# Kernel tuning notes

Hardware: AMD Instinct MI355X
Metric: run time of the kernel (lower is better)

The kernel has to match this reference:

```python
import jax, jax.numpy as jnp
import numpy as np

C_M, C_Z, C_H = 256, 128, 32
EPS = 1e-3      # outer-product-mean normalization eps
LN_EPS = 1e-5   # LayerNorm eps (torch default)


def setup_inputs() -> dict:
    key = jax.random.key(0)
    ks = jax.random.split(key, 8)
    B, S, R = 1, 128, 256
    m = jax.random.normal(ks[0], (B, S, R, C_M), dtype=jnp.float32)
    mask = jnp.ones((B, S, R), dtype=jnp.float32)
    ln_g = jnp.ones((C_M,), dtype=jnp.float32)
    ln_b = jnp.zeros((C_M,), dtype=jnp.float32)
    w1 = jax.random.normal(ks[1], (C_M, C_H), dtype=jnp.float32) * (1.0 / np.sqrt(C_M))
    b1 = jnp.zeros((C_H,), dtype=jnp.float32)
    w2 = jax.random.normal(ks[2], (C_M, C_H), dtype=jnp.float32) * (1.0 / np.sqrt(C_M))
    b2 = jnp.zeros((C_H,), dtype=jnp.float32)
    # linear_out uses init='final' (zeros) in training; use small random for a nontrivial baseline
    w_out = jax.random.normal(ks[3], (C_H * C_H, C_Z), dtype=jnp.float32) * 0.02
    b_out = jnp.zeros((C_Z,), dtype=jnp.float32)
    return {"m": m, "mask": mask, "ln_g": ln_g, "ln_b": ln_b,
            "w1": w1, "b1": b1, "w2": w2, "b2": b2,
            "w_out": w_out, "b_out": b_out}


def reference(m, mask, ln_g, ln_b, w1, b1, w2, b2, w_out, b_out):
    # LayerNorm over c_m
    mu = jnp.mean(m, axis=-1, keepdims=True)
    var = jnp.mean(jnp.square(m - mu), axis=-1, keepdims=True)
    mn = (m - mu) * jax.lax.rsqrt(var + LN_EPS) * ln_g + ln_b

    msk = mask[..., None]                       # [B,S,R,1]
    a = (mn @ w1 + b1) * msk                    # [B,S,R,h]
    b = (mn @ w2 + b2) * msk                    # [B,S,R,h]
    a = jnp.swapaxes(a, -2, -3)                 # [B,R,S,h]
    b = jnp.swapaxes(b, -2, -3)                 # [B,R,S,h]

    # outer product mean over the MSA (seq) dim: [B,R,R,h,h]
    outer = jnp.einsum('...isc,...jse->...ijce', a, b)
    outer = outer.reshape(*outer.shape[:-2], C_H * C_H)  # [B,R,R,h*h]
    outer = outer @ w_out + b_out               # [B,R,R,c_z]

    # normalization: pairwise count of valid MSA rows
    norm = jnp.einsum('...sia,...sja->...ija', msk, msk)  # [B,R,R,1]
    return outer / (EPS + norm)
```

## Files before the change

kernel.cpp:

```cpp
#include <hip/hip_runtime.h>

#define R   256
#define S   128
#define CM  256
#define CH  32
#define CZ  128

typedef __attribute__((ext_vector_type(8))) short short8;
typedef __attribute__((ext_vector_type(4))) float f32x4;
typedef unsigned short ushort_t;

__device__ inline ushort_t f2bf(float f) {
    union { float f; unsigned u; } v; v.f = f;
    unsigned u = v.u;
    unsigned r = u + 0x7FFF + ((u >> 16) & 1);
    return (ushort_t)(r >> 16);
}

__global__ __launch_bounds__(256) void k_prep(
    const float* __restrict__ mask, const float* __restrict__ w_out,
    const float* __restrict__ w1, const float* __restrict__ w2,
    float* __restrict__ scale, ushort_t* __restrict__ WTp,
    ushort_t* __restrict__ WcatT) {
    __shared__ float red[4][64];
    int b = blockIdx.x, t = threadIdx.x;
    if (b < 1024) {
        int i = b >> 2, jq = b & 3;
        int jl = t & 63, wv = t >> 6;
        int j = jq * 64 + jl;
        const float* mi = mask + (size_t)(wv * 32) * R + i;
        const float* mj = mask + (size_t)(wv * 32) * R + j;
        float acc = 0.f;
        #pragma unroll
        for (int s = 0; s < 32; ++s) acc += mi[s * R] * mj[s * R];
        red[wv][jl] = acc;
        __syncthreads();
        if (t < 64) {
            float v = red[0][t] + red[1][t] + red[2][t] + red[3][t];
            scale[(size_t)i * R + jq * 64 + t] = 1.0f / (1e-3f + v);
        }
    } else if (b < 1152) {
        int z = b - 1024;
        #pragma unroll
        for (int q = 0; q < 4; ++q) {
            int k2 = q * 256 + t;
            int e = k2 >> 5, c = k2 & 31;
            WTp[(size_t)z * 1024 + k2] = f2bf(w_out[(size_t)(c * 32 + e) * CZ + z]);
        }
    } else {
        int ch = b - 1152, k = t;
        const float* w = (ch < CH) ? w1 : w2;
        WcatT[(size_t)ch * CM + k] = f2bf(w[(size_t)k * CH + (ch & 31)]);
    }
}

__global__ __launch_bounds__(256) void k_lnproj(
    const float* __restrict__ m, const float* __restrict__ mask,
    const float* __restrict__ g, const float* __restrict__ beta,
    const float* __restrict__ b1, const float* __restrict__ b2,
    const ushort_t* __restrict__ WcatT,
    ushort_t* __restrict__ Abig, ushort_t* __restrict__ BbigT) {
    __shared__ ushort_t mnL[64 * CM];
    int t = threadIdx.x;
    int sg = blockIdx.x & 7, rg = blockIdx.x >> 3;
    int s0 = sg * 16, r0 = rg * 4;

    int ml = t >> 2, part = t & 3;
    int r_l = ml >> 4, s_l = ml & 15;
    size_t p = (size_t)(s0 + s_l) * R + (r0 + r_l);
    const float4* row = (const float4*)(m + p * CM + part * 64);
    float4 x[16];
    float sum = 0.f, sq = 0.f;
    #pragma unroll
    for (int i = 0; i < 16; ++i) {
        x[i] = row[i];
        sum += x[i].x + x[i].y + x[i].z + x[i].w;
        sq  += x[i].x * x[i].x + x[i].y * x[i].y
             + x[i].z * x[i].z + x[i].w * x[i].w;
    }
    sum += __shfl_xor(sum, 1); sum += __shfl_xor(sum, 2);
    sq  += __shfl_xor(sq, 1);  sq  += __shfl_xor(sq, 2);
    float mean = sum * (1.0f / CM);
    float var  = sq * (1.0f / CM) - mean * mean;
    float inv  = rsqrtf(var + 1e-5f);
    const float4* g4 = (const float4*)(g + part * 64);
    const float4* be4 = (const float4*)(beta + part * 64);
    #pragma unroll
    for (int c8 = 0; c8 < 8; ++c8) {
        float4 a = x[2 * c8], b = x[2 * c8 + 1];
        float4 ga = g4[2 * c8], gb = g4[2 * c8 + 1];
        float4 ba = be4[2 * c8], bb = be4[2 * c8 + 1];
        union { ushort_t u[8]; uint4 v; } pk;
        pk.u[0] = f2bf((a.x - mean) * inv * ga.x + ba.x);
        pk.u[1] = f2bf((a.y - mean) * inv * ga.y + ba.y);
        pk.u[2] = f2bf((a.z - mean) * inv * ga.z + ba.z);
        pk.u[3] = f2bf((a.w - mean) * inv * ga.w + ba.w);
        pk.u[4] = f2bf((b.x - mean) * inv * gb.x + bb.x);
        pk.u[5] = f2bf((b.y - mean) * inv * gb.y + bb.y);
        pk.u[6] = f2bf((b.z - mean) * inv * gb.z + bb.z);
        pk.u[7] = f2bf((b.w - mean) * inv * gb.w + bb.w);
        int ck = part * 8 + c8;
        int phys = ck ^ (ml & 15);
        *(uint4*)&mnL[ml * CM + phys * 8] = pk.v;
    }

    int w = t >> 6, lane = t & 63, quad = lane >> 4, l15 = lane & 15;
    int ch = w * 16 + l15;
    short8 bfrs[8];
    #pragma unroll
    for (int ks = 0; ks < 8; ++ks)
        bfrs[ks] = *(const short8*)&WcatT[(size_t)ch * CM + (ks * 4 + quad) * 8];
    __syncthreads();

    f32x4 acc[4];
    #pragma unroll
    for (int a = 0; a < 4; a++) acc[a] = (f32x4)(0.f);
    #pragma unroll
    for (int ks = 0; ks < 8; ++ks) {
        int cb = ks * 4 + quad;
        #pragma unroll
        for (int mt = 0; mt < 4; ++mt) {
            int mm = mt * 16 + l15;
            short8 afr = *(const short8*)&mnL[mm * CM + ((cb ^ l15) << 3)];
            acc[mt] = __builtin_amdgcn_mfma_f32_16x16x32_bf16(afr, bfrs[ks], acc[mt], 0, 0, 0);
        }
    }

    int c = ch & 31;
    float bias = (ch < CH) ? b1[c] : b2[c];
    ushort_t* dst = (ch < CH) ? Abig : BbigT;
    #pragma unroll
    for (int mt = 0; mt < 4; ++mt) {
        int r = r0 + mt;
        union { ushort_t u[4]; uint2 v; } pk;
        #pragma unroll
        for (int reg = 0; reg < 4; ++reg) {
            int s = s0 + quad * 4 + reg;
            float mv = mask[(size_t)s * R + r];
            pk.u[reg] = f2bf((acc[mt][reg] + bias) * mv);
        }
        *(uint2*)&dst[((size_t)r * CH + c) * S + s0 + quad * 4] = pk.v;
    }
}

__global__ __launch_bounds__(512, 4) void k_fuse(
    const ushort_t* __restrict__ Abig, const ushort_t* __restrict__ BbigT,
    const ushort_t* __restrict__ WTp, const float* __restrict__ b_out,
    const float* __restrict__ scale, float* __restrict__ out) {
    __shared__ ushort_t oc[64 * 128];
    __shared__ ushort_t shB[2][32 * 128];
    int t = threadIdx.x;
    int w = t >> 6, lane = t & 63, quad = lane >> 4, l15 = lane & 15;
    int ib = blockIdx.x >> 5, jb = blockIdx.x & 31;
    int i_g = ib * 8 + w;
    int jj = l15 & 7, elb = l15 >> 3;

    short8 af[2][4];
    #pragma unroll
    for (int mt = 0; mt < 2; ++mt)
        #pragma unroll
        for (int ks = 0; ks < 4; ++ks)
            af[mt][ks] = *(const short8*)
                &Abig[((size_t)i_g * 32 + mt * 16 + l15) * S + ks * 32 + quad * 8];

    int r2 = t >> 4, ck = t & 15;
    const ushort_t* gB = BbigT
        + ((size_t)jb * 256 + (r2 & 7) * 32 + (r2 >> 3)) * S + ck * 8;
    ushort_t* bdst[2];
    bdst[0] = &shB[0][r2 * 128 + ((ck ^ (r2 & 15)) << 3)];
    bdst[1] = &shB[1][r2 * 128 + ((ck ^ (r2 & 15)) << 3)];
    uint4 breg = *(const uint4*)&gB[0];

    const ushort_t* Wp = WTp + (size_t)(w * 16 + l15) * 1024 + quad * 8;
    short8 wcur[4], wnxt[4];
    #pragma unroll
    for (int k = 0; k < 4; ++k) wcur[k] = *(const short8*)&Wp[k * 32];

    int pwr = w * 8 + jj;

    f32x4 acc2[4];
    #pragma unroll
    for (int pt = 0; pt < 4; ++pt) acc2[pt] = (f32x4)(0.f);

    for (int ec = 0; ec < 8; ++ec) {
        int buf = ec & 1;
        *(uint4*)bdst[buf] = breg;
        __syncthreads();

        if (ec < 7) {
            breg = *(const uint4*)&gB[(ec + 1) * 512];
            #pragma unroll
            for (int k = 0; k < 4; ++k)
                wnxt[k] = *(const short8*)&Wp[(ec + 1) * 128 + k * 32];
        }

        f32x4 acc1[2][2];
        #pragma unroll
        for (int a = 0; a < 2; a++)
            #pragma unroll
            for (int b = 0; b < 2; b++) acc1[a][b] = (f32x4)(0.f);
        #pragma unroll
        for (int ks = 0; ks < 4; ++ks) {
            int chq = ks * 4 + quad;
            int r20 = elb * 8 + jj;
            int r21 = r20 + 16;
            short8 bf0 = *(const short8*)
                &shB[buf][r20 * 128 + ((chq ^ (r20 & 15)) << 3)];
            short8 bf1 = *(const short8*)
                &shB[buf][r21 * 128 + ((chq ^ (r21 & 15)) << 3)];
            #pragma unroll
            for (int mt = 0; mt < 2; ++mt) {
                acc1[mt][0] = __builtin_amdgcn_mfma_f32_16x16x32_bf16(
                    af[mt][ks], bf0, acc1[mt][0], 0, 0, 0);
                acc1[mt][1] = __builtin_amdgcn_mfma_f32_16x16x32_bf16(
                    af[mt][ks], bf1, acc1[mt][1], 0, 0, 0);
            }
        }
        #pragma unroll
        for (int mt = 0; mt < 2; ++mt) {
            int c00 = mt * 16 + quad * 4;
            #pragma unroll
            for (int nt = 0; nt < 2; ++nt) {
                int el = nt * 2 + elb;
                int k2l = el * 32 + c00;
                int cc = k2l >> 3;
                union { ushort_t u[4]; uint2 v; } pk;
                #pragma unroll
                for (int reg = 0; reg < 4; ++reg)
                    pk.u[reg] = f2bf(acc1[mt][nt][reg]);
                *(uint2*)((char*)oc + pwr * 256 + ((cc ^ (pwr & 7)) << 4)
                          + ((k2l & 7) << 1)) = pk.v;
            }
        }
        __syncthreads();
        #pragma unroll
        for (int ksl = 0; ksl < 4; ++ksl) {
            short8 wf = wcur[ksl];
            #pragma unroll
            for (int pt = 0; pt < 4; ++pt) {
                int pp = pt * 16 + l15;
                int cc = ksl * 4 + quad;
                short8 of = *(const short8*)
                    ((const char*)oc + pp * 256 + ((cc ^ (pp & 7)) << 4));
                acc2[pt] = __builtin_amdgcn_mfma_f32_16x16x32_bf16(
                    of, wf, acc2[pt], 0, 0, 0);
            }
        }
        #pragma unroll
        for (int k = 0; k < 4; ++k) wcur[k] = wnxt[k];
    }

    float bz = b_out[w * 16 + l15];
    #pragma unroll
    for (int pt = 0; pt < 4; ++pt) {
        #pragma unroll
        for (int reg = 0; reg < 4; ++reg) {
            int pp = pt * 16 + quad * 4 + reg;
            int pg = (ib * 8 + (pp >> 3)) * R + jb * 8 + (pp & 7);
            out[(size_t)pg * CZ + w * 16 + l15] = (acc2[pt][reg] + bz) * scale[pg];
        }
    }
}

extern "C" void kernel_launch(void* const* d_in, const int* in_sizes, int n_in,
                              void* d_out, int out_size, void* d_ws, size_t ws_size,
                              hipStream_t stream) {
    const float* m    = (const float*)d_in[0];
    const float* mask = (const float*)d_in[1];
    const float* g    = (const float*)d_in[2];
    const float* be   = (const float*)d_in[3];
    const float* w1   = (const float*)d_in[4];
    const float* b1   = (const float*)d_in[5];
    const float* w2   = (const float*)d_in[6];
    const float* b2   = (const float*)d_in[7];
    const float* wo   = (const float*)d_in[8];
    const float* bo   = (const float*)d_in[9];
    float* out = (float*)d_out;

    char* ws = (char*)d_ws;
    ushort_t* Abig  = (ushort_t*)ws;
    ushort_t* BbigT = Abig + (size_t)R * CH * S;
    ushort_t* WTp   = BbigT + (size_t)R * CH * S;
    ushort_t* WcatT = WTp + (size_t)CZ * CH * CH;
    float*    scale = (float*)(WcatT + (size_t)64 * CM);

    k_prep<<<1216, 256, 0, stream>>>(mask, wo, w1, w2, scale, WTp, WcatT);
    k_lnproj<<<512, 256, 0, stream>>>(m, mask, g, be, b1, b2, WcatT, Abig, BbigT);
    k_fuse<<<1024, 512, 0, stream>>>(Abig, BbigT, WTp, bo, scale, out);
}
```

Measured before the change: 158.3 us.

## Restructure fused outer-product GEMM tiling and fold mask-norm/W_out prep into lnproj

The mask-count normalization and w_out transpose work moves out of the prep kernel into extra blocks of the LN/projection kernel, so the first launch shrinks to a tiny w1/w2 conversion. In the fused kernel, B fragments are now loaded directly from global memory into registers instead of being staged through shared memory. The outer-product staging buffer is double-buffered, and the second GEMM is retiled so each wave computes 32 rows by 32 output channels with W fragments streamed from global memory. The 4-blocks-per-SM occupancy hint is dropped. The aim is fewer barriers and less LDS traffic, at the cost of more global loads and higher register pressure.

```diff
diff --git a/kernel.cpp b/kernel.cpp
--- a/kernel.cpp
+++ b/kernel.cpp
@@ -17,15 +17,39 @@
     return (ushort_t)(r >> 16);
 }
 
-__global__ __launch_bounds__(256) void k_prep(
-    const float* __restrict__ mask, const float* __restrict__ w_out,
+__global__ __launch_bounds__(256) void k_prepW(
     const float* __restrict__ w1, const float* __restrict__ w2,
-    float* __restrict__ scale, ushort_t* __restrict__ WTp,
     ushort_t* __restrict__ WcatT) {
-    __shared__ float red[4][64];
-    int b = blockIdx.x, t = threadIdx.x;
-    if (b < 1024) {
-        int i = b >> 2, jq = b & 3;
+    int ch = blockIdx.x, k = threadIdx.x;
+    const float* w = (ch < CH) ? w1 : w2;
+    WcatT[(size_t)ch * CM + k] = f2bf(w[(size_t)k * CH + (ch & 31)]);
+}
+
+__global__ __launch_bounds__(256) void k_lnproj(
+    const float* __restrict__ m, const float* __restrict__ mask,
+    const float* __restrict__ g, const float* __restrict__ beta,
+    const float* __restrict__ b1, const float* __restrict__ b2,
+    const ushort_t* __restrict__ WcatT, const float* __restrict__ w_out,
+    ushort_t* __restrict__ Abig, ushort_t* __restrict__ BbigT,
+    float* __restrict__ scale, ushort_t* __restrict__ WTp) {
+    __shared__ ushort_t mnL[64 * CM];
+    int t = threadIdx.x;
+    int b = blockIdx.x;
+
+    if (b >= 1536) {
+        int z = b - 1536;
+        #pragma unroll
+        for (int q = 0; q < 4; ++q) {
+            int k2 = q * 256 + t;
+            int e = k2 >> 5, c = k2 & 31;
+            WTp[(size_t)z * 1024 + k2] = f2bf(w_out[(size_t)(c * 32 + e) * CZ + z]);
+        }
+        return;
+    }
+    if (b >= 512) {
+        float* red = (float*)mnL;
+        int bb = b - 512;
+        int i = bb >> 2, jq = bb & 3;
         int jl = t & 63, wv = t >> 6;
         int j = jq * 64 + jl;
         const float* mi = mask + (size_t)(wv * 32) * R + i;
@@ -33,36 +57,16 @@
         float acc = 0.f;
         #pragma unroll
         for (int s = 0; s < 32; ++s) acc += mi[s * R] * mj[s * R];
-        red[wv][jl] = acc;
+        red[wv * 64 + jl] = acc;
         __syncthreads();
         if (t < 64) {
-            float v = red[0][t] + red[1][t] + red[2][t] + red[3][t];
+            float v = red[t] + red[64 + t] + red[128 + t] + red[192 + t];
             scale[(size_t)i * R + jq * 64 + t] = 1.0f / (1e-3f + v);
         }
-    } else if (b < 1152) {
-        int z = b - 1024;
-        #pragma unroll
-        for (int q = 0; q < 4; ++q) {
-            int k2 = q * 256 + t;
-            int e = k2 >> 5, c = k2 & 31;
-            WTp[(size_t)z * 1024 + k2] = f2bf(w_out[(size_t)(c * 32 + e) * CZ + z]);
-        }
-    } else {
-        int ch = b - 1152, k = t;
-        const float* w = (ch < CH) ? w1 : w2;
-        WcatT[(size_t)ch * CM + k] = f2bf(w[(size_t)k * CH + (ch & 31)]);
-    }
-}
-
-__global__ __launch_bounds__(256) void k_lnproj(
-    const float* __restrict__ m, const float* __restrict__ mask,
-    const float* __restrict__ g, const float* __restrict__ beta,
-    const float* __restrict__ b1, const float* __restrict__ b2,
-    const ushort_t* __restrict__ WcatT,
-    ushort_t* __restrict__ Abig, ushort_t* __restrict__ BbigT) {
-    __shared__ ushort_t mnL[64 * CM];
-    int t = threadIdx.x;
-    int sg = blockIdx.x & 7, rg = blockIdx.x >> 3;
+        return;
+    }
+
+    int sg = b & 7, rg = b >> 3;
     int s0 = sg * 16, r0 = rg * 4;
 
     int ml = t >> 2, part = t & 3;
@@ -87,7 +91,7 @@
     const float4* be4 = (const float4*)(beta + part * 64);
     #pragma unroll
     for (int c8 = 0; c8 < 8; ++c8) {
-        float4 a = x[2 * c8], b = x[2 * c8 + 1];
+        float4 a = x[2 * c8], bq = x[2 * c8 + 1];
         float4 ga = g4[2 * c8], gb = g4[2 * c8 + 1];
         float4 ba = be4[2 * c8], bb = be4[2 * c8 + 1];
         union { ushort_t u[8]; uint4 v; } pk;
@@ -95,10 +99,10 @@
         pk.u[1] = f2bf((a.y - mean) * inv * ga.y + ba.y);
         pk.u[2] = f2bf((a.z - mean) * inv * ga.z + ba.z);
         pk.u[3] = f2bf((a.w - mean) * inv * ga.w + ba.w);
-        pk.u[4] = f2bf((b.x - mean) * inv * gb.x + bb.x);
-        pk.u[5] = f2bf((b.y - mean) * inv * gb.y + bb.y);
-        pk.u[6] = f2bf((b.z - mean) * inv * gb.z + bb.z);
-        pk.u[7] = f2bf((b.w - mean) * inv * gb.w + bb.w);
+        pk.u[4] = f2bf((bq.x - mean) * inv * gb.x + bb.x);
+        pk.u[5] = f2bf((bq.y - mean) * inv * gb.y + bb.y);
+        pk.u[6] = f2bf((bq.z - mean) * inv * gb.z + bb.z);
+        pk.u[7] = f2bf((bq.w - mean) * inv * gb.w + bb.w);
         int ck = part * 8 + c8;
         int phys = ck ^ (ml & 15);
         *(uint4*)&mnL[ml * CM + phys * 8] = pk.v;
@@ -143,12 +147,11 @@
     }
 }
 
-__global__ __launch_bounds__(512, 4) void k_fuse(
+__global__ __launch_bounds__(512) void k_fuse(
     const ushort_t* __restrict__ Abig, const ushort_t* __restrict__ BbigT,
     const ushort_t* __restrict__ WTp, const float* __restrict__ b_out,
     const float* __restrict__ scale, float* __restrict__ out) {
-    __shared__ ushort_t oc[64 * 128];
-    __shared__ ushort_t shB[2][32 * 128];
+    __shared__ ushort_t oc[2][64 * 128];
     int t = threadIdx.x;
     int w = t >> 6, lane = t & 63, quad = lane >> 4, l15 = lane & 15;
     int ib = blockIdx.x >> 5, jb = blockIdx.x & 31;
@@ -163,57 +166,41 @@
             af[mt][ks] = *(const short8*)
                 &Abig[((size_t)i_g * 32 + mt * 16 + l15) * S + ks * 32 + quad * 8];
 
-    int r2 = t >> 4, ck = t & 15;
-    const ushort_t* gB = BbigT
-        + ((size_t)jb * 256 + (r2 & 7) * 32 + (r2 >> 3)) * S + ck * 8;
-    ushort_t* bdst[2];
-    bdst[0] = &shB[0][r2 * 128 + ((ck ^ (r2 & 15)) << 3)];
-    bdst[1] = &shB[1][r2 * 128 + ((ck ^ (r2 & 15)) << 3)];
-    uint4 breg = *(const uint4*)&gB[0];
-
-    const ushort_t* Wp = WTp + (size_t)(w * 16 + l15) * 1024 + quad * 8;
-    short8 wcur[4], wnxt[4];
-    #pragma unroll
-    for (int k = 0; k < 4; ++k) wcur[k] = *(const short8*)&Wp[k * 32];
-
+    const ushort_t* gB = BbigT + ((size_t)jb * 256 + jj * 32 + elb) * S + quad * 8;
+
+    const ushort_t* Wp = WTp + ((size_t)((w & 3) * 32) + l15) * 1024 + quad * 8;
+
+    int ph = w >> 2;
     int pwr = w * 8 + jj;
 
-    f32x4 acc2[4];
-    #pragma unroll
-    for (int pt = 0; pt < 4; ++pt) acc2[pt] = (f32x4)(0.f);
-
+    f32x4 acc2[2][2];
+    #pragma unroll
+    for (int a = 0; a < 2; ++a)
+        #pragma unroll
+        for (int zt = 0; zt < 2; ++zt) acc2[a][zt] = (f32x4)(0.f);
+
+    short8 bcur[2][4];
+    #pragma unroll
+    for (int nt = 0; nt < 2; ++nt)
+        #pragma unroll
+        for (int ks = 0; ks < 4; ++ks)
+            bcur[nt][ks] = *(const short8*)&gB[(size_t)(nt * 2) * S + ks * 32];
+
+    #pragma unroll
     for (int ec = 0; ec < 8; ++ec) {
-        int buf = ec & 1;
-        *(uint4*)bdst[buf] = breg;
-        __syncthreads();
-
-        if (ec < 7) {
-            breg = *(const uint4*)&gB[(ec + 1) * 512];
-            #pragma unroll
-            for (int k = 0; k < 4; ++k)
-                wnxt[k] = *(const short8*)&Wp[(ec + 1) * 128 + k * 32];
-        }
-
         f32x4 acc1[2][2];
         #pragma unroll
         for (int a = 0; a < 2; a++)
             #pragma unroll
-            for (int b = 0; b < 2; b++) acc1[a][b] = (f32x4)(0.f);
+            for (int bq = 0; bq < 2; bq++) acc1[a][bq] = (f32x4)(0.f);
         #pragma unroll
         for (int ks = 0; ks < 4; ++ks) {
-            int chq = ks * 4 + quad;
-            int r20 = elb * 8 + jj;
-            int r21 = r20 + 16;
-            short8 bf0 = *(const short8*)
-                &shB[buf][r20 * 128 + ((chq ^ (r20 & 15)) << 3)];
-            short8 bf1 = *(const short8*)
-                &shB[buf][r21 * 128 + ((chq ^ (r21 & 15)) << 3)];
             #pragma unroll
             for (int mt = 0; mt < 2; ++mt) {
                 acc1[mt][0] = __builtin_amdgcn_mfma_f32_16x16x32_bf16(
-                    af[mt][ks], bf0, acc1[mt][0], 0, 0, 0);
+                    af[mt][ks], bcur[0][ks], acc1[mt][0], 0, 0, 0);
                 acc1[mt][1] = __builtin_amdgcn_mfma_f32_16x16x32_bf16(
-                    af[mt][ks], bf1, acc1[mt][1], 0, 0, 0);
+                    af[mt][ks], bcur[1][ks], acc1[mt][1], 0, 0, 0);
             }
         }
         #pragma unroll
@@ -228,36 +215,52 @@
                 #pragma unroll
                 for (int reg = 0; reg < 4; ++reg)
                     pk.u[reg] = f2bf(acc1[mt][nt][reg]);
-                *(uint2*)((char*)oc + pwr * 256 + ((cc ^ (pwr & 7)) << 4)
-                          + ((k2l & 7) << 1)) = pk.v;
+                *(uint2*)((char*)oc[ec & 1] + pwr * 256
+                          + ((cc ^ (pwr & 15)) << 4) + ((k2l & 7) << 1)) = pk.v;
             }
         }
         __syncthreads();
+
+        if (ec < 7) {
+            #pragma unroll
+            for (int nt = 0; nt < 2; ++nt)
+                #pragma unroll
+                for (int ks = 0; ks < 4; ++ks)
+                    bcur[nt][ks] = *(const short8*)
+                        &gB[(size_t)((ec + 1) * 4 + nt * 2) * S + ks * 32];
+        }
+
         #pragma unroll
         for (int ksl = 0; ksl < 4; ++ksl) {
-            short8 wf = wcur[ksl];
-            #pragma unroll
-            for (int pt = 0; pt < 4; ++pt) {
-                int pp = pt * 16 + l15;
-                int cc = ksl * 4 + quad;
+            short8 wf0 = *(const short8*)&Wp[ec * 128 + ksl * 32];
+            short8 wf1 = *(const short8*)&Wp[16 * 1024 + ec * 128 + ksl * 32];
+            #pragma unroll
+            for (int mtile = 0; mtile < 2; ++mtile) {
+                int pp = ph * 32 + mtile * 16 + l15;
+                int cc2 = ksl * 4 + quad;
                 short8 of = *(const short8*)
-                    ((const char*)oc + pp * 256 + ((cc ^ (pp & 7)) << 4));
-                acc2[pt] = __builtin_amdgcn_mfma_f32_16x16x32_bf16(
-                    of, wf, acc2[pt], 0, 0, 0);
+                    ((const char*)oc[ec & 1] + pp * 256 + ((cc2 ^ (pp & 15)) << 4));
+                acc2[mtile][0] = __builtin_amdgcn_mfma_f32_16x16x32_bf16(
+                    of, wf0, acc2[mtile][0], 0, 0, 0);
+                acc2[mtile][1] = __builtin_amdgcn_mfma_f32_16x16x32_bf16(
+                    of, wf1, acc2[mtile][1], 0, 0, 0);
             }
         }
-        #pragma unroll
-        for (int k = 0; k < 4; ++k) wcur[k] = wnxt[k];
-    }
-
-    float bz = b_out[w * 16 + l15];
-    #pragma unroll
-    for (int pt = 0; pt < 4; ++pt) {
+    }
+
+    float bz0 = b_out[(w & 3) * 32 + l15];
+    float bz1 = b_out[(w & 3) * 32 + 16 + l15];
+    #pragma unroll
+    for (int mtile = 0; mtile < 2; ++mtile) {
         #pragma unroll
         for (int reg = 0; reg < 4; ++reg) {
-            int pp = pt * 16 + quad * 4 + reg;
-            int pg = (ib * 8 + (pp >> 3)) * R + jb * 8 + (pp & 7);
-            out[(size_t)pg * CZ + w * 16 + l15] = (acc2[pt][reg] + bz) * scale[pg];
+            int pq = ph * 32 + mtile * 16 + quad * 4 + reg;
+            int pg = (ib * 8 + (pq >> 3)) * R + jb * 8 + (pq & 7);
+            float sc = scale[pg];
+            out[(size_t)pg * CZ + (w & 3) * 32 + l15]
+                = (acc2[mtile][0][reg] + bz0) * sc;
+            out[(size_t)pg * CZ + (w & 3) * 32 + 16 + l15]
+                = (acc2[mtile][1][reg] + bz1) * sc;
         }
     }
 }
@@ -284,7 +287,8 @@
     ushort_t* WcatT = WTp + (size_t)CZ * CH * CH;
     float*    scale = (float*)(WcatT + (size_t)64 * CM);
 
-    k_prep<<<1216, 256, 0, stream>>>(mask, wo, w1, w2, scale, WTp, WcatT);
-    k_lnproj<<<512, 256, 0, stream>>>(m, mask, g, be, b1, b2, WcatT, Abig, BbigT);
+    k_prepW<<<64, 256, 0, stream>>>(w1, w2, WcatT);
+    k_lnproj<<<1664, 256, 0, stream>>>(m, mask, g, be, b1, b2, WcatT, wo,
+                                       Abig, BbigT, scale, WTp);
     k_fuse<<<1024, 512, 0, stream>>>(Abig, BbigT, WTp, bo, scale, out);
 }
```

After: 238.6 us. 50.7% more time.

## Fold prep kernel into LN-projection launch and load fused weights directly

Applied to the files above, without the earlier changes.

Merges the mask-count, w_out transpose and LN+projection work into one launch by dispatching on block index, which removes one kernel launch and its dependency gap. The separate w1/w2 transposed bf16 copy is dropped; each LN block now converts the projection weights from fp32 with strided global reads. In the fused kernel the register double-buffer for w_out fragments is removed in favour of direct loads inside the loop. This saves registers but may expose load latency, and the strided per-block weight conversion adds redundant global traffic.

```diff
diff --git a/kernel.cpp b/kernel.cpp
--- a/kernel.cpp
+++ b/kernel.cpp
@@ -17,15 +17,32 @@
     return (ushort_t)(r >> 16);
 }
 
-__global__ __launch_bounds__(256) void k_prep(
-    const float* __restrict__ mask, const float* __restrict__ w_out,
+__global__ __launch_bounds__(256) void k_lnproj(
+    const float* __restrict__ m, const float* __restrict__ mask,
+    const float* __restrict__ g, const float* __restrict__ beta,
+    const float* __restrict__ b1, const float* __restrict__ b2,
     const float* __restrict__ w1, const float* __restrict__ w2,
-    float* __restrict__ scale, ushort_t* __restrict__ WTp,
-    ushort_t* __restrict__ WcatT) {
-    __shared__ float red[4][64];
-    int b = blockIdx.x, t = threadIdx.x;
-    if (b < 1024) {
-        int i = b >> 2, jq = b & 3;
+    const float* __restrict__ w_out,
+    ushort_t* __restrict__ Abig, ushort_t* __restrict__ BbigT,
+    float* __restrict__ scale, ushort_t* __restrict__ WTp) {
+    __shared__ ushort_t mnL[64 * CM];
+    int t = threadIdx.x;
+    int b = blockIdx.x;
+
+    if (b >= 1536) {
+        int z = b - 1536;
+        #pragma unroll
+        for (int q = 0; q < 4; ++q) {
+            int k2 = q * 256 + t;
+            int e = k2 >> 5, c = k2 & 31;
+            WTp[(size_t)z * 1024 + k2] = f2bf(w_out[(size_t)(c * 32 + e) * CZ + z]);
+        }
+        return;
+    }
+    if (b >= 512) {
+        float* red = (float*)mnL;
+        int bb = b - 512;
+        int i = bb >> 2, jq = bb & 3;
         int jl = t & 63, wv = t >> 6;
         int j = jq * 64 + jl;
         const float* mi = mask + (size_t)(wv * 32) * R + i;
@@ -33,36 +50,16 @@
         float acc = 0.f;
         #pragma unroll
         for (int s = 0; s < 32; ++s) acc += mi[s * R] * mj[s * R];
-        red[wv][jl] = acc;
+        red[wv * 64 + jl] = acc;
         __syncthreads();
         if (t < 64) {
-            float v = red[0][t] + red[1][t] + red[2][t] + red[3][t];
+            float v = red[t] + red[64 + t] + red[128 + t] + red[192 + t];
             scale[(size_t)i * R + jq * 64 + t] = 1.0f / (1e-3f + v);
         }
-    } else if (b < 1152) {
-        int z = b - 1024;
-        #pragma unroll
-        for (int q = 0; q < 4; ++q) {
-            int k2 = q * 256 + t;
-            int e = k2 >> 5, c = k2 & 31;
-            WTp[(size_t)z * 1024 + k2] = f2bf(w_out[(size_t)(c * 32 + e) * CZ + z]);
-        }
-    } else {
-        int ch = b - 1152, k = t;
-        const float* w = (ch < CH) ? w1 : w2;
-        WcatT[(size_t)ch * CM + k] = f2bf(w[(size_t)k * CH + (ch & 31)]);
-    }
-}
-
-__global__ __launch_bounds__(256) void k_lnproj(
-    const float* __restrict__ m, const float* __restrict__ mask,
-    const float* __restrict__ g, const float* __restrict__ beta,
-    const float* __restrict__ b1, const float* __restrict__ b2,
-    const ushort_t* __restrict__ WcatT,
-    ushort_t* __restrict__ Abig, ushort_t* __restrict__ BbigT) {
-    __shared__ ushort_t mnL[64 * CM];
-    int t = threadIdx.x;
-    int sg = blockIdx.x & 7, rg = blockIdx.x >> 3;
+        return;
+    }
+
+    int sg = b & 7, rg = b >> 3;
     int s0 = sg * 16, r0 = rg * 4;
 
     int ml = t >> 2, part = t & 3;
@@ -87,7 +84,7 @@
     const float4* be4 = (const float4*)(beta + part * 64);
     #pragma unroll
     for (int c8 = 0; c8 < 8; ++c8) {
-        float4 a = x[2 * c8], b = x[2 * c8 + 1];
+        float4 a = x[2 * c8], bq = x[2 * c8 + 1];
         float4 ga = g4[2 * c8], gb = g4[2 * c8 + 1];
         float4 ba = be4[2 * c8], bb = be4[2 * c8 + 1];
         union { ushort_t u[8]; uint4 v; } pk;
@@ -95,10 +92,10 @@
         pk.u[1] = f2bf((a.y - mean) * inv * ga.y + ba.y);
         pk.u[2] = f2bf((a.z - mean) * inv * ga.z + ba.z);
         pk.u[3] = f2bf((a.w - mean) * inv * ga.w + ba.w);
-        pk.u[4] = f2bf((b.x - mean) * inv * gb.x + bb.x);
-        pk.u[5] = f2bf((b.y - mean) * inv * gb.y + bb.y);
-        pk.u[6] = f2bf((b.z - mean) * inv * gb.z + bb.z);
-        pk.u[7] = f2bf((b.w - mean) * inv * gb.w + bb.w);
+        pk.u[4] = f2bf((bq.x - mean) * inv * gb.x + bb.x);
+        pk.u[5] = f2bf((bq.y - mean) * inv * gb.y + bb.y);
+        pk.u[6] = f2bf((bq.z - mean) * inv * gb.z + bb.z);
+        pk.u[7] = f2bf((bq.w - mean) * inv * gb.w + bb.w);
         int ck = part * 8 + c8;
         int phys = ck ^ (ml & 15);
         *(uint4*)&mnL[ml * CM + phys * 8] = pk.v;
@@ -106,10 +103,18 @@
 
     int w = t >> 6, lane = t & 63, quad = lane >> 4, l15 = lane & 15;
     int ch = w * 16 + l15;
+    const float* wsrc = (ch < CH) ? w1 : w2;
+    int cidx = ch & 31;
     short8 bfrs[8];
     #pragma unroll
-    for (int ks = 0; ks < 8; ++ks)
-        bfrs[ks] = *(const short8*)&WcatT[(size_t)ch * CM + (ks * 4 + quad) * 8];
+    for (int ks = 0; ks < 8; ++ks) {
+        int cb = ks * 4 + quad;
+        union { ushort_t u[8]; short8 v; } pw;
+        #pragma unroll
+        for (int e = 0; e < 8; ++e)
+            pw.u[e] = f2bf(wsrc[(size_t)(cb * 8 + e) * CH + cidx]);
+        bfrs[ks] = pw.v;
+    }
     __syncthreads();
 
     f32x4 acc[4];
@@ -172,10 +177,6 @@
     uint4 breg = *(const uint4*)&gB[0];
 
     const ushort_t* Wp = WTp + (size_t)(w * 16 + l15) * 1024 + quad * 8;
-    short8 wcur[4], wnxt[4];
-    #pragma unroll
-    for (int k = 0; k < 4; ++k) wcur[k] = *(const short8*)&Wp[k * 32];
-
     int pwr = w * 8 + jj;
 
     f32x4 acc2[4];
@@ -185,14 +186,8 @@
     for (int ec = 0; ec < 8; ++ec) {
         int buf = ec & 1;
         *(uint4*)bdst[buf] = breg;
+        if (ec < 7) breg = *(const uint4*)&gB[(ec + 1) * 512];
         __syncthreads();
-
-        if (ec < 7) {
-            breg = *(const uint4*)&gB[(ec + 1) * 512];
-            #pragma unroll
-            for (int k = 0; k < 4; ++k)
-                wnxt[k] = *(const short8*)&Wp[(ec + 1) * 128 + k * 32];
-        }
 
         f32x4 acc1[2][2];
         #pragma unroll
@@ -235,7 +230,7 @@
         __syncthreads();
         #pragma unroll
         for (int ksl = 0; ksl < 4; ++ksl) {
-            short8 wf = wcur[ksl];
+            short8 wf = *(const short8*)&Wp[ec * 128 + ksl * 32];
             #pragma unroll
             for (int pt = 0; pt < 4; ++pt) {
                 int pp = pt * 16 + l15;
@@ -246,8 +241,6 @@
                     of, wf, acc2[pt], 0, 0, 0);
             }
         }
-        #pragma unroll
-        for (int k = 0; k < 4; ++k) wcur[k] = wnxt[k];
     }
 
     float bz = b_out[w * 16 + l15];
@@ -281,10 +274,9 @@
     ushort_t* Abig  = (ushort_t*)ws;
     ushort_t* BbigT = Abig + (size_t)R * CH * S;
     ushort_t* WTp   = BbigT + (size_t)R * CH * S;
-    ushort_t* WcatT = WTp + (size_t)CZ * CH * CH;
-    float*    scale = (float*)(WcatT + (size_t)64 * CM);
-
-    k_prep<<<1216, 256, 0, stream>>>(mask, wo, w1, w2, scale, WTp, WcatT);
-    k_lnproj<<<512, 256, 0, stream>>>(m, mask, g, be, b1, b2, WcatT, Abig, BbigT);
+    float*    scale = (float*)(WTp + (size_t)CZ * CH * CH);
+
+    k_lnproj<<<1664, 256, 0, stream>>>(m, mask, g, be, b1, b2, w1, w2, wo,
+                                       Abig, BbigT, scale, WTp);
     k_fuse<<<1024, 512, 0, stream>>>(Abig, BbigT, WTp, bo, scale, out);
 }
```

Result: no change. 156.3 us (-1.3%).
